# Kernel tuning notes

Measured on AMD Instinct MI355X. Metric: run time of the kernel, lower is better.

Reference implementation:

```python
import jax, jax.numpy as jnp
import numpy as np

BS, N, DE, DX = 16, 256, 64, 256
BIG = 100000.0


def setup_inputs() -> dict:
    key = jax.random.key(0)
    k1, k2, k3, k4 = jax.random.split(key, 4)
    E = jax.random.normal(k1, (BS, N, N, DE), dtype=jnp.float32)
    e_mask2 = jax.random.uniform(k2, (BS, 1, N, 1)) < 0.8
    fan_in = 4 * DE
    bound = 1.0 / np.sqrt(fan_in)
    W = jax.random.uniform(k3, (DX, fan_in), minval=-bound, maxval=bound, dtype=jnp.float32)
    b = jax.random.uniform(k4, (DX,), minval=-bound, maxval=bound, dtype=jnp.float32)
    return {"E": E, "e_mask2": e_mask2, "W": W, "b": b}


def reference(E, e_mask2, W, b):
    bs, n, _, de = E.shape
    mask = jnp.broadcast_to(e_mask2, (bs, n, n, de)).astype(E.dtype)  # bs,n,n,de
    imask = 1.0 - mask
    denom = mask.sum(axis=2)                       # bs,n,de
    m = E.sum(axis=2) / denom                      # (faithful: unmasked sum / mask count)
    mi = (E + BIG * imask).min(axis=2)             # masked min
    ma = (E - BIG * imask).max(axis=2)             # masked max
    std = (((E - m[:, :, None, :]) ** 2) * mask).sum(axis=2) / denom
    z = jnp.concatenate((m, mi, ma, std), axis=2)  # bs,n,4*de
    return jnp.einsum('bnf,df->bnd', z, W) + b     # bs,n,dx
```

## Files before the change

### kernel.cpp

```cpp
#include <hip/hip_runtime.h>
#include <cstdint>
#include <cstddef>

#define BSZ 16
#define NN  256
#define DE  64
#define DXX 256
#define FAN (4 * DE)
#define IB  4
#define RB  16

__global__ __launch_bounds__(256) void prep_kernel(
    const uint8_t* __restrict__ raw, const float* __restrict__ W,
    float* __restrict__ WT, float* __restrict__ maskf)
{
    const int t   = threadIdx.x;
    const int blk = blockIdx.x;
    if (blk < FAN) {
        WT[blk * DXX + t] = W[t * FAN + blk];
    } else {
        __shared__ int det[2];
        if (t == 0) { det[0] = 0; det[1] = 0; }
        __syncthreads();
        int s1 = 0, s23 = 0;
        const uint8_t* p = raw + t * 16;
        #pragma unroll
        for (int u = 0; u < 16; ++u) {
            int v = (int)p[u];
            int m4 = u & 3;
            if (m4 == 1) s1 += v; else if (m4 >= 2) s23 += v;
        }
        if (s1)  atomicAdd(&det[0], s1);
        if (s23) atomicAdd(&det[1], s23);
        __syncthreads();
        const int kind = (det[1] == 0) ? 1 : ((det[0] == 0) ? 2 : 0);
        for (int idx = t; idx < BSZ * NN; idx += 256) {
            float mv;
            if (kind == 1)      mv = (((const int*)(const void*)raw)[idx] != 0) ? 1.f : 0.f;
            else if (kind == 2) mv = (((const float*)(const void*)raw)[idx] != 0.f) ? 1.f : 0.f;
            else                mv = (raw[idx] != 0) ? 1.f : 0.f;
            maskf[idx] = mv;
        }
    }
}

__global__ __launch_bounds__(256, 4) void k1_stats(
    const float* __restrict__ E, const float* __restrict__ maskf,
    float* __restrict__ zout)
{
    __shared__ float m_lds[NN];
    __shared__ float cpart[4];
    __shared__ float partial[4][16][20];

    const int t    = threadIdx.x;
    const int g0   = blockIdx.x * IB;
    const int b    = g0 >> 8;
    const int wv   = t >> 6;
    const int lane = t & 63;

    float mv = maskf[b * NN + t];
    m_lds[t] = mv;
    unsigned long long bal = __ballot(mv != 0.f);
    if (lane == 0) cpart[wv] = (float)__popcll(bal);
    __syncthreads();
    const float inv_cnt = 1.0f / (cpart[0] + cpart[1] + cpart[2] + cpart[3]);

    const int dq = t & 15;
    const int jb = t >> 4;

    float mk[16];
    #pragma unroll
    for (int k = 0; k < 16; ++k) mk[k] = m_lds[jb + 16 * k];

    const float* base0 = E + (size_t)g0 * (NN * DE) + (size_t)jb * DE + 4 * dq;

    #define LD(P, K) (*(const float4*)((P) + (size_t)(K) * (16 * DE)))
    float4 A0, A1, A2, A3, B0, B1, B2, B3;
    A0 = LD(base0, 0); A1 = LD(base0, 1); A2 = LD(base0, 2); A3 = LD(base0, 3);

    for (int r = 0; r < IB; ++r) {
        const float* baser = base0 + (size_t)r * (NN * DE);

        float s[4]  = {0.f, 0.f, 0.f, 0.f};
        float ms[4] = {0.f, 0.f, 0.f, 0.f};
        float q[4]  = {0.f, 0.f, 0.f, 0.f};
        float mi[4] = {1e30f, 1e30f, 1e30f, 1e30f};
        float ma[4] = {-1e30f, -1e30f, -1e30f, -1e30f};

        #define CONS1(V, KK) { \
            float mkv = mk[KK]; \
            bool on = (mkv != 0.f); \
            float4 v = V; \
            s[0] += v.x; s[1] += v.y; s[2] += v.z; s[3] += v.w; \
            ms[0] = fmaf(mkv, v.x, ms[0]); ms[1] = fmaf(mkv, v.y, ms[1]); \
            ms[2] = fmaf(mkv, v.z, ms[2]); ms[3] = fmaf(mkv, v.w, ms[3]); \
            q[0] = fmaf(mkv * v.x, v.x, q[0]); q[1] = fmaf(mkv * v.y, v.y, q[1]); \
            q[2] = fmaf(mkv * v.z, v.z, q[2]); q[3] = fmaf(mkv * v.w, v.w, q[3]); \
            mi[0] = fminf(mi[0], on ? v.x : 1e30f); mi[1] = fminf(mi[1], on ? v.y : 1e30f); \
            mi[2] = fminf(mi[2], on ? v.z : 1e30f); mi[3] = fminf(mi[3], on ? v.w : 1e30f); \
            ma[0] = fmaxf(ma[0], on ? v.x : -1e30f); ma[1] = fmaxf(ma[1], on ? v.y : -1e30f); \
            ma[2] = fmaxf(ma[2], on ? v.z : -1e30f); ma[3] = fmaxf(ma[3], on ? v.w : -1e30f); \
        }

        B0 = LD(baser, 4);  B1 = LD(baser, 5);  B2 = LD(baser, 6);  B3 = LD(baser, 7);
        CONS1(A0, 0) CONS1(A1, 1) CONS1(A2, 2) CONS1(A3, 3)
        A0 = LD(baser, 8);  A1 = LD(baser, 9);  A2 = LD(baser, 10); A3 = LD(baser, 11);
        CONS1(B0, 4) CONS1(B1, 5) CONS1(B2, 6) CONS1(B3, 7)
        B0 = LD(baser, 12); B1 = LD(baser, 13); B2 = LD(baser, 14); B3 = LD(baser, 15);
        CONS1(A0, 8) CONS1(A1, 9) CONS1(A2, 10) CONS1(A3, 11)
        if (r < IB - 1) {
            const float* basen = baser + (NN * DE);
            A0 = LD(basen, 0); A1 = LD(basen, 1); A2 = LD(basen, 2); A3 = LD(basen, 3);
        }
        CONS1(B0, 12) CONS1(B1, 13) CONS1(B2, 14) CONS1(B3, 15)
        #undef CONS1

        #pragma unroll
        for (int c = 0; c < 4; ++c) {
            s[c]  += __shfl_xor(s[c], 16);  s[c]  += __shfl_xor(s[c], 32);
            ms[c] += __shfl_xor(ms[c], 16); ms[c] += __shfl_xor(ms[c], 32);
            q[c]  += __shfl_xor(q[c], 16);  q[c]  += __shfl_xor(q[c], 32);
            mi[c] = fminf(mi[c], __shfl_xor(mi[c], 16));
            mi[c] = fminf(mi[c], __shfl_xor(mi[c], 32));
            ma[c] = fmaxf(ma[c], __shfl_xor(ma[c], 16));
            ma[c] = fmaxf(ma[c], __shfl_xor(ma[c], 32));
        }

        if (lane < 16) {
            float* p = partial[wv][lane];
            #pragma unroll
            for (int c = 0; c < 4; ++c) {
                p[c]      = s[c];
                p[4 + c]  = ms[c];
                p[8 + c]  = q[c];
                p[12 + c] = mi[c];
                p[16 + c] = ma[c];
            }
        }
        __syncthreads();

        if (t < 64) {
            const int d = t, dq2 = d >> 2, c = d & 3;
            float ss = 0.f, mss = 0.f, mq = 0.f, lmi = 1e30f, lma = -1e30f;
            #pragma unroll
            for (int w = 0; w < 4; ++w) {
                const float* p = partial[w][dq2];
                ss  += p[c];
                mss += p[4 + c];
                mq  += p[8 + c];
                lmi  = fminf(lmi, p[12 + c]);
                lma  = fmaxf(lma, p[16 + c]);
            }
            float m    = ss * inv_cnt;
            float stdv = mq * inv_cnt - 2.0f * m * (mss * inv_cnt) + m * m;
            float* zr = zout + (size_t)(g0 + r) * FAN;
            zr[d]       = m;
            zr[64 + d]  = lmi;
            zr[128 + d] = lma;
            zr[192 + d] = stdv;
        }
        __syncthreads();
    }
    #undef LD
}

__global__ __launch_bounds__(256, 2) void k2_gemm(
    const float* __restrict__ zin, const float* __restrict__ WT,
    const float* __restrict__ bias, float* __restrict__ out)
{
    __shared__ float  z_s[RB][FAN];
    __shared__ float4 part_c[4][RB][64];

    const int t    = threadIdx.x;
    const int r0   = blockIdx.x * RB;
    const int wv   = t >> 6;
    const int lane = t & 63;

    #pragma unroll
    for (int i = 0; i < RB; ++i)
        z_s[i][t] = zin[(size_t)(r0 + i) * FAN + t];
    __syncthreads();

    float4 acc[RB];
    #pragma unroll
    for (int i = 0; i < RB; ++i) acc[i] = make_float4(0.f, 0.f, 0.f, 0.f);

    const float4* WT4 = (const float4*)WT;
    int f0 = 64 * wv;
    #pragma unroll 2
    for (int fg = 0; fg < 16; ++fg, f0 += 4) {
        float4 w0 = WT4[(size_t)(f0 + 0) * 64 + lane];
        float4 w1 = WT4[(size_t)(f0 + 1) * 64 + lane];
        float4 w2 = WT4[(size_t)(f0 + 2) * 64 + lane];
        float4 w3 = WT4[(size_t)(f0 + 3) * 64 + lane];
        #pragma unroll
        for (int i = 0; i < RB; ++i) {
            float4 z4 = *(const float4*)(&z_s[i][f0]);
            acc[i].x = fmaf(z4.x, w0.x, fmaf(z4.y, w1.x, fmaf(z4.z, w2.x, fmaf(z4.w, w3.x, acc[i].x))));
            acc[i].y = fmaf(z4.x, w0.y, fmaf(z4.y, w1.y, fmaf(z4.z, w2.y, fmaf(z4.w, w3.y, acc[i].y))));
            acc[i].z = fmaf(z4.x, w0.z, fmaf(z4.y, w1.z, fmaf(z4.z, w2.z, fmaf(z4.w, w3.z, acc[i].z))));
            acc[i].w = fmaf(z4.x, w0.w, fmaf(z4.y, w1.w, fmaf(z4.z, w2.w, fmaf(z4.w, w3.w, acc[i].w))));
        }
    }
    #pragma unroll
    for (int i = 0; i < RB; ++i) part_c[wv][i][lane] = acc[i];
    __syncthreads();

    #pragma unroll
    for (int pass = 0; pass < 4; ++pass) {
        const int idx = pass * 256 + t;
        const int row = idx >> 6, l2 = idx & 63;
        float4 p0 = part_c[0][row][l2], p1 = part_c[1][row][l2];
        float4 p2 = part_c[2][row][l2], p3 = part_c[3][row][l2];
        float4 bv = *(const float4*)(bias + 4 * l2);
        float4 o;
        o.x = p0.x + p1.x + p2.x + p3.x + bv.x;
        o.y = p0.y + p1.y + p2.y + p3.y + bv.y;
        o.z = p0.z + p1.z + p2.z + p3.z + bv.z;
        o.w = p0.w + p1.w + p2.w + p3.w + bv.w;
        *(float4*)(out + (size_t)(r0 + row) * DXX + 4 * l2) = o;
    }
}

__global__ __launch_bounds__(256, 4) void etox_legacy(
    const float* __restrict__ E, const uint8_t* __restrict__ raw,
    const float* __restrict__ W, const float* __restrict__ bias,
    float* __restrict__ out)
{
    __shared__ float m_lds[NN];
    __shared__ int   det[2];
    __shared__ float cpart[4];
    __shared__ float partial[4][16][20];
    __shared__ float z_lds[IB][FAN];

    const int t    = threadIdx.x;
    const int g0   = blockIdx.x * IB;
    const int b    = g0 >> 8;
    const int wv   = t >> 6;
    const int lane = t & 63;

    if (t == 0) { det[0] = 0; det[1] = 0; }
    int s1 = 0, s23 = 0;
    {
        const uint8_t* p = raw + t * 16;
        #pragma unroll
        for (int u = 0; u < 16; ++u) {
            int v = (int)p[u];
            int m4 = u & 3;
            if (m4 == 1) s1 += v; else if (m4 >= 2) s23 += v;
        }
    }
    __syncthreads();
    if (s1)  atomicAdd(&det[0], s1);
    if (s23) atomicAdd(&det[1], s23);
    __syncthreads();
    const int kind = (det[1] == 0) ? 1 : ((det[0] == 0) ? 2 : 0);
    float mv;
    {
        int idx = b * NN + t;
        if (kind == 1)      mv = (((const int*)(const void*)raw)[idx] != 0) ? 1.f : 0.f;
        else if (kind == 2) mv = (((const float*)(const void*)raw)[idx] != 0.f) ? 1.f : 0.f;
        else                mv = (raw[idx] != 0) ? 1.f : 0.f;
    }
    m_lds[t] = mv;
    unsigned long long bal = __ballot(mv != 0.f);
    if (lane == 0) cpart[wv] = (float)__popcll(bal);
    __syncthreads();
    const float inv_cnt = 1.0f / (cpart[0] + cpart[1] + cpart[2] + cpart[3]);

    const int dq = t & 15;
    const int jb = t >> 4;
    const float* base0 = E + (size_t)g0 * (NN * DE) + (size_t)jb * DE + 4 * dq;

    #define LD(P, K) (*(const float4*)((P) + (size_t)(K) * (16 * DE)))
    float4 A0, A1, A2, A3, B0, B1, B2, B3;
    A0 = LD(base0, 0); A1 = LD(base0, 1); A2 = LD(base0, 2); A3 = LD(base0, 3);

    for (int r = 0; r < IB; ++r) {
        const float* baser = base0 + (size_t)r * (NN * DE);
        float s[4]  = {0.f, 0.f, 0.f, 0.f};
        float ms[4] = {0.f, 0.f, 0.f, 0.f};
        float q[4]  = {0.f, 0.f, 0.f, 0.f};
        float mi[4] = {1e30f, 1e30f, 1e30f, 1e30f};
        float ma[4] = {-1e30f, -1e30f, -1e30f, -1e30f};

        #define CONS1(V, KK) { \
            float mkv = m_lds[jb + 16 * (KK)]; \
            bool on = (mkv != 0.f); \
            float4 v = V; \
            s[0] += v.x; s[1] += v.y; s[2] += v.z; s[3] += v.w; \
            ms[0] = fmaf(mkv, v.x, ms[0]); ms[1] = fmaf(mkv, v.y, ms[1]); \
            ms[2] = fmaf(mkv, v.z, ms[2]); ms[3] = fmaf(mkv, v.w, ms[3]); \
            q[0] = fmaf(mkv * v.x, v.x, q[0]); q[1] = fmaf(mkv * v.y, v.y, q[1]); \
            q[2] = fmaf(mkv * v.z, v.z, q[2]); q[3] = fmaf(mkv * v.w, v.w, q[3]); \
            mi[0] = fminf(mi[0], on ? v.x : 1e30f); mi[1] = fminf(mi[1], on ? v.y : 1e30f); \
            mi[2] = fminf(mi[2], on ? v.z : 1e30f); mi[3] = fminf(mi[3], on ? v.w : 1e30f); \
            ma[0] = fmaxf(ma[0], on ? v.x : -1e30f); ma[1] = fmaxf(ma[1], on ? v.y : -1e30f); \
            ma[2] = fmaxf(ma[2], on ? v.z : -1e30f); ma[3] = fmaxf(ma[3], on ? v.w : -1e30f); \
        }

        B0 = LD(baser, 4);  B1 = LD(baser, 5);  B2 = LD(baser, 6);  B3 = LD(baser, 7);
        CONS1(A0, 0) CONS1(A1, 1) CONS1(A2, 2) CONS1(A3, 3)
        A0 = LD(baser, 8);  A1 = LD(baser, 9);  A2 = LD(baser, 10); A3 = LD(baser, 11);
        CONS1(B0, 4) CONS1(B1, 5) CONS1(B2, 6) CONS1(B3, 7)
        B0 = LD(baser, 12); B1 = LD(baser, 13); B2 = LD(baser, 14); B3 = LD(baser, 15);
        CONS1(A0, 8) CONS1(A1, 9) CONS1(A2, 10) CONS1(A3, 11)
        if (r < IB - 1) {
            const float* basen = baser + (NN * DE);
            A0 = LD(basen, 0); A1 = LD(basen, 1); A2 = LD(basen, 2); A3 = LD(basen, 3);
        }
        CONS1(B0, 12) CONS1(B1, 13) CONS1(B2, 14) CONS1(B3, 15)
        #undef CONS1

        #pragma unroll
        for (int c = 0; c < 4; ++c) {
            s[c]  += __shfl_xor(s[c], 16);  s[c]  += __shfl_xor(s[c], 32);
            ms[c] += __shfl_xor(ms[c], 16); ms[c] += __shfl_xor(ms[c], 32);
            q[c]  += __shfl_xor(q[c], 16);  q[c]  += __shfl_xor(q[c], 32);
            mi[c] = fminf(mi[c], __shfl_xor(mi[c], 16));
            mi[c] = fminf(mi[c], __shfl_xor(mi[c], 32));
            ma[c] = fmaxf(ma[c], __shfl_xor(ma[c], 16));
            ma[c] = fmaxf(ma[c], __shfl_xor(ma[c], 32));
        }

        if (lane < 16) {
            float* p = partial[wv][lane];
            #pragma unroll
            for (int c = 0; c < 4; ++c) {
                p[c] = s[c]; p[4+c] = ms[c]; p[8+c] = q[c];
                p[12+c] = mi[c]; p[16+c] = ma[c];
            }
        }
        __syncthreads();

        if (t < 64) {
            const int d = t, dq2 = d >> 2, c = d & 3;
            float ss = 0.f, mss = 0.f, mq = 0.f, lmi = 1e30f, lma = -1e30f;
            #pragma unroll
            for (int w = 0; w < 4; ++w) {
                const float* p = partial[w][dq2];
                ss += p[c]; mss += p[4+c]; mq += p[8+c];
                lmi = fminf(lmi, p[12+c]); lma = fmaxf(lma, p[16+c]);
            }
            float m    = ss * inv_cnt;
            float stdv = mq * inv_cnt - 2.0f * m * (mss * inv_cnt) + m * m;
            z_lds[r][d] = m; z_lds[r][64+d] = lmi; z_lds[r][128+d] = lma; z_lds[r][192+d] = stdv;
        }
        __syncthreads();
    }
    #undef LD

    float acc0, acc1, acc2, acc3;
    {
        float bv = bias[t];
        acc0 = bv; acc1 = bv; acc2 = bv; acc3 = bv;
    }
    const float4* Wrow = (const float4*)(W + (size_t)t * FAN);
    #pragma unroll 8
    for (int f4 = 0; f4 < 64; ++f4) {
        float4 w4 = Wrow[f4];
        int f = 4 * f4;
        acc0 += z_lds[0][f]*w4.x + z_lds[0][f+1]*w4.y + z_lds[0][f+2]*w4.z + z_lds[0][f+3]*w4.w;
        acc1 += z_lds[1][f]*w4.x + z_lds[1][f+1]*w4.y + z_lds[1][f+2]*w4.z + z_lds[1][f+3]*w4.w;
        acc2 += z_lds[2][f]*w4.x + z_lds[2][f+1]*w4.y + z_lds[2][f+2]*w4.z + z_lds[2][f+3]*w4.w;
        acc3 += z_lds[3][f]*w4.x + z_lds[3][f+1]*w4.y + z_lds[3][f+2]*w4.z + z_lds[3][f+3]*w4.w;
    }
    out[(size_t)(g0 + 0) * DXX + t] = acc0;
    out[(size_t)(g0 + 1) * DXX + t] = acc1;
    out[(size_t)(g0 + 2) * DXX + t] = acc2;
    out[(size_t)(g0 + 3) * DXX + t] = acc3;
}

extern "C" void kernel_launch(void* const* d_in, const int* in_sizes, int n_in,
                              void* d_out, int out_size, void* d_ws, size_t ws_size,
                              hipStream_t stream) {
    const float*   E    = (const float*)d_in[0];
    const uint8_t* mraw = (const uint8_t*)d_in[1];
    const float*   W    = (const float*)d_in[2];
    const float*   bias = (const float*)d_in[3];
    float*         out  = (float*)d_out;

    const size_t wt_n   = (size_t)FAN * DXX;
    const size_t mask_n = (size_t)BSZ * NN;
    const size_t z_n    = (size_t)BSZ * NN * FAN;
    const size_t need   = (wt_n + mask_n + z_n) * sizeof(float);

    if (ws_size >= need) {
        float* WT    = (float*)d_ws;
        float* maskf = WT + wt_n;
        float* zbuf  = maskf + mask_n;
        prep_kernel<<<FAN + 1, 256, 0, stream>>>(mraw, W, WT, maskf);
        k1_stats<<<(BSZ * NN) / IB, 256, 0, stream>>>(E, maskf, zbuf);
        k2_gemm<<<(BSZ * NN) / RB, 256, 0, stream>>>(zbuf, WT, bias, out);
    } else {
        etox_legacy<<<(BSZ * NN) / IB, 256, 0, stream>>>(E, mraw, W, bias, out);
    }
}
```

Before: 77.54 us.

## Fuse stats and GEMM into one producer-consumer kernel with a GEMV warp

Merges the stats kernel and the separate GEMM kernel into a single kernel with 320 threads: four waves compute the per-row statistics into LDS while a fifth consumer wave computes the matrix-vector product for the previous row, overlapping the two stages. This removes the global round-trip of the z buffer and one kernel launch. In exchange, every block re-reads the full transposed weight matrix (256 KB) from cache per row instead of amortizing it over 16 rows. Mask values are now read from LDS per element rather than held in registers.

```diff
diff --git a/kernel.cpp b/kernel.cpp
--- a/kernel.cpp
+++ b/kernel.cpp
@@ -8,7 +8,6 @@
 #define DXX 256
 #define FAN (4 * DE)
 #define IB  4
-#define RB  16
 
 __global__ __launch_bounds__(256) void prep_kernel(
     const uint8_t* __restrict__ raw, const float* __restrict__ W,
@@ -44,98 +43,124 @@
     }
 }
 
-__global__ __launch_bounds__(256, 4) void k1_stats(
+__global__ __launch_bounds__(320, 5) void etox_pc(
     const float* __restrict__ E, const float* __restrict__ maskf,
-    float* __restrict__ zout)
+    const float* __restrict__ WT, const float* __restrict__ bias,
+    float* __restrict__ out)
 {
     __shared__ float m_lds[NN];
     __shared__ float cpart[4];
     __shared__ float partial[4][16][20];
-
-    const int t    = threadIdx.x;
-    const int g0   = blockIdx.x * IB;
-    const int b    = g0 >> 8;
-    const int wv   = t >> 6;
-    const int lane = t & 63;
-
-    float mv = maskf[b * NN + t];
-    m_lds[t] = mv;
-    unsigned long long bal = __ballot(mv != 0.f);
-    if (lane == 0) cpart[wv] = (float)__popcll(bal);
+    __shared__ float z_lds[IB][FAN];
+
+    const int t      = threadIdx.x;
+    const int g0     = blockIdx.x * IB;
+    const int b      = g0 >> 8;
+    const int wv     = t >> 6;
+    const int lane   = t & 63;
+    const bool cons  = (t >= 256);
+
+    if (!cons) {
+        float mv = maskf[b * NN + t];
+        m_lds[t] = mv;
+        unsigned long long bal = __ballot(mv != 0.f);
+        if (lane == 0) cpart[wv] = (float)__popcll(bal);
+    }
     __syncthreads();
     const float inv_cnt = 1.0f / (cpart[0] + cpart[1] + cpart[2] + cpart[3]);
 
+    const float4* WT4 = (const float4*)WT;
+    float4 bv4 = make_float4(0.f, 0.f, 0.f, 0.f);
+    if (cons) bv4 = *(const float4*)(bias + 4 * lane);
+
     const int dq = t & 15;
     const int jb = t >> 4;
-
-    float mk[16];
-    #pragma unroll
-    for (int k = 0; k < 16; ++k) mk[k] = m_lds[jb + 16 * k];
-
     const float* base0 = E + (size_t)g0 * (NN * DE) + (size_t)jb * DE + 4 * dq;
 
     #define LD(P, K) (*(const float4*)((P) + (size_t)(K) * (16 * DE)))
     float4 A0, A1, A2, A3, B0, B1, B2, B3;
-    A0 = LD(base0, 0); A1 = LD(base0, 1); A2 = LD(base0, 2); A3 = LD(base0, 3);
+    if (!cons) { A0 = LD(base0, 0); A1 = LD(base0, 1); A2 = LD(base0, 2); A3 = LD(base0, 3); }
+
+    #define CONS_MV(RZ, DEST_ROW) { \
+        float4 acc = make_float4(0.f, 0.f, 0.f, 0.f); \
+        _Pragma("unroll 4") \
+        for (int f = 0; f < FAN; f += 4) { \
+            float4 w0 = WT4[(size_t)(f + 0) * 64 + lane]; \
+            float4 w1 = WT4[(size_t)(f + 1) * 64 + lane]; \
+            float4 w2 = WT4[(size_t)(f + 2) * 64 + lane]; \
+            float4 w3 = WT4[(size_t)(f + 3) * 64 + lane]; \
+            float4 z4 = *(const float4*)(&z_lds[RZ][f]); \
+            acc.x = fmaf(z4.x, w0.x, fmaf(z4.y, w1.x, fmaf(z4.z, w2.x, fmaf(z4.w, w3.x, acc.x)))); \
+            acc.y = fmaf(z4.x, w0.y, fmaf(z4.y, w1.y, fmaf(z4.z, w2.y, fmaf(z4.w, w3.y, acc.y)))); \
+            acc.z = fmaf(z4.x, w0.z, fmaf(z4.y, w1.z, fmaf(z4.z, w2.z, fmaf(z4.w, w3.z, acc.z)))); \
+            acc.w = fmaf(z4.x, w0.w, fmaf(z4.y, w1.w, fmaf(z4.z, w2.w, fmaf(z4.w, w3.w, acc.w)))); \
+        } \
+        acc.x += bv4.x; acc.y += bv4.y; acc.z += bv4.z; acc.w += bv4.w; \
+        *(float4*)(out + (size_t)(g0 + (DEST_ROW)) * DXX + 4 * lane) = acc; \
+    }
 
     for (int r = 0; r < IB; ++r) {
-        const float* baser = base0 + (size_t)r * (NN * DE);
-
-        float s[4]  = {0.f, 0.f, 0.f, 0.f};
-        float ms[4] = {0.f, 0.f, 0.f, 0.f};
-        float q[4]  = {0.f, 0.f, 0.f, 0.f};
-        float mi[4] = {1e30f, 1e30f, 1e30f, 1e30f};
-        float ma[4] = {-1e30f, -1e30f, -1e30f, -1e30f};
-
-        #define CONS1(V, KK) { \
-            float mkv = mk[KK]; \
-            bool on = (mkv != 0.f); \
-            float4 v = V; \
-            s[0] += v.x; s[1] += v.y; s[2] += v.z; s[3] += v.w; \
-            ms[0] = fmaf(mkv, v.x, ms[0]); ms[1] = fmaf(mkv, v.y, ms[1]); \
-            ms[2] = fmaf(mkv, v.z, ms[2]); ms[3] = fmaf(mkv, v.w, ms[3]); \
-            q[0] = fmaf(mkv * v.x, v.x, q[0]); q[1] = fmaf(mkv * v.y, v.y, q[1]); \
-            q[2] = fmaf(mkv * v.z, v.z, q[2]); q[3] = fmaf(mkv * v.w, v.w, q[3]); \
-            mi[0] = fminf(mi[0], on ? v.x : 1e30f); mi[1] = fminf(mi[1], on ? v.y : 1e30f); \
-            mi[2] = fminf(mi[2], on ? v.z : 1e30f); mi[3] = fminf(mi[3], on ? v.w : 1e30f); \
-            ma[0] = fmaxf(ma[0], on ? v.x : -1e30f); ma[1] = fmaxf(ma[1], on ? v.y : -1e30f); \
-            ma[2] = fmaxf(ma[2], on ? v.z : -1e30f); ma[3] = fmaxf(ma[3], on ? v.w : -1e30f); \
-        }
-
-        B0 = LD(baser, 4);  B1 = LD(baser, 5);  B2 = LD(baser, 6);  B3 = LD(baser, 7);
-        CONS1(A0, 0) CONS1(A1, 1) CONS1(A2, 2) CONS1(A3, 3)
-        A0 = LD(baser, 8);  A1 = LD(baser, 9);  A2 = LD(baser, 10); A3 = LD(baser, 11);
-        CONS1(B0, 4) CONS1(B1, 5) CONS1(B2, 6) CONS1(B3, 7)
-        B0 = LD(baser, 12); B1 = LD(baser, 13); B2 = LD(baser, 14); B3 = LD(baser, 15);
-        CONS1(A0, 8) CONS1(A1, 9) CONS1(A2, 10) CONS1(A3, 11)
-        if (r < IB - 1) {
-            const float* basen = baser + (NN * DE);
-            A0 = LD(basen, 0); A1 = LD(basen, 1); A2 = LD(basen, 2); A3 = LD(basen, 3);
-        }
-        CONS1(B0, 12) CONS1(B1, 13) CONS1(B2, 14) CONS1(B3, 15)
-        #undef CONS1
-
-        #pragma unroll
-        for (int c = 0; c < 4; ++c) {
-            s[c]  += __shfl_xor(s[c], 16);  s[c]  += __shfl_xor(s[c], 32);
-            ms[c] += __shfl_xor(ms[c], 16); ms[c] += __shfl_xor(ms[c], 32);
-            q[c]  += __shfl_xor(q[c], 16);  q[c]  += __shfl_xor(q[c], 32);
-            mi[c] = fminf(mi[c], __shfl_xor(mi[c], 16));
-            mi[c] = fminf(mi[c], __shfl_xor(mi[c], 32));
-            ma[c] = fmaxf(ma[c], __shfl_xor(ma[c], 16));
-            ma[c] = fmaxf(ma[c], __shfl_xor(ma[c], 32));
-        }
-
-        if (lane < 16) {
-            float* p = partial[wv][lane];
+        if (!cons) {
+            const float* baser = base0 + (size_t)r * (NN * DE);
+
+            float s[4]  = {0.f, 0.f, 0.f, 0.f};
+            float ms[4] = {0.f, 0.f, 0.f, 0.f};
+            float q[4]  = {0.f, 0.f, 0.f, 0.f};
+            float mi[4] = {1e30f, 1e30f, 1e30f, 1e30f};
+            float ma[4] = {-1e30f, -1e30f, -1e30f, -1e30f};
+
+            #define CONS1(V, KK) { \
+                float mk = m_lds[jb + 16 * (KK)]; \
+                bool on = (mk != 0.f); \
+                float4 v = V; \
+                s[0] += v.x; s[1] += v.y; s[2] += v.z; s[3] += v.w; \
+                ms[0] = fmaf(mk, v.x, ms[0]); ms[1] = fmaf(mk, v.y, ms[1]); \
+                ms[2] = fmaf(mk, v.z, ms[2]); ms[3] = fmaf(mk, v.w, ms[3]); \
+                q[0] = fmaf(mk * v.x, v.x, q[0]); q[1] = fmaf(mk * v.y, v.y, q[1]); \
+                q[2] = fmaf(mk * v.z, v.z, q[2]); q[3] = fmaf(mk * v.w, v.w, q[3]); \
+                mi[0] = fminf(mi[0], on ? v.x : 1e30f); mi[1] = fminf(mi[1], on ? v.y : 1e30f); \
+                mi[2] = fminf(mi[2], on ? v.z : 1e30f); mi[3] = fminf(mi[3], on ? v.w : 1e30f); \
+                ma[0] = fmaxf(ma[0], on ? v.x : -1e30f); ma[1] = fmaxf(ma[1], on ? v.y : -1e30f); \
+                ma[2] = fmaxf(ma[2], on ? v.z : -1e30f); ma[3] = fmaxf(ma[3], on ? v.w : -1e30f); \
+            }
+
+            B0 = LD(baser, 4);  B1 = LD(baser, 5);  B2 = LD(baser, 6);  B3 = LD(baser, 7);
+            CONS1(A0, 0) CONS1(A1, 1) CONS1(A2, 2) CONS1(A3, 3)
+            A0 = LD(baser, 8);  A1 = LD(baser, 9);  A2 = LD(baser, 10); A3 = LD(baser, 11);
+            CONS1(B0, 4) CONS1(B1, 5) CONS1(B2, 6) CONS1(B3, 7)
+            B0 = LD(baser, 12); B1 = LD(baser, 13); B2 = LD(baser, 14); B3 = LD(baser, 15);
+            CONS1(A0, 8) CONS1(A1, 9) CONS1(A2, 10) CONS1(A3, 11)
+            if (r < IB - 1) {
+                const float* basen = baser + (NN * DE);
+                A0 = LD(basen, 0); A1 = LD(basen, 1); A2 = LD(basen, 2); A3 = LD(basen, 3);
+            }
+            CONS1(B0, 12) CONS1(B1, 13) CONS1(B2, 14) CONS1(B3, 15)
+            #undef CONS1
+
             #pragma unroll
             for (int c = 0; c < 4; ++c) {
-                p[c]      = s[c];
-                p[4 + c]  = ms[c];
-                p[8 + c]  = q[c];
-                p[12 + c] = mi[c];
-                p[16 + c] = ma[c];
-            }
+                s[c]  += __shfl_xor(s[c], 16);  s[c]  += __shfl_xor(s[c], 32);
+                ms[c] += __shfl_xor(ms[c], 16); ms[c] += __shfl_xor(ms[c], 32);
+                q[c]  += __shfl_xor(q[c], 16);  q[c]  += __shfl_xor(q[c], 32);
+                mi[c] = fminf(mi[c], __shfl_xor(mi[c], 16));
+                mi[c] = fminf(mi[c], __shfl_xor(mi[c], 32));
+                ma[c] = fmaxf(ma[c], __shfl_xor(ma[c], 16));
+                ma[c] = fmaxf(ma[c], __shfl_xor(ma[c], 32));
+            }
+
+            if (lane < 16) {
+                float* p = partial[wv][lane];
+                #pragma unroll
+                for (int c = 0; c < 4; ++c) {
+                    p[c]      = s[c];
+                    p[4 + c]  = ms[c];
+                    p[8 + c]  = q[c];
+                    p[12 + c] = mi[c];
+                    p[16 + c] = ma[c];
+                }
+            }
+        } else {
+            if (r > 0) CONS_MV(r - 1, r - 1)
         }
         __syncthreads();
 
@@ -153,73 +178,17 @@
             }
             float m    = ss * inv_cnt;
             float stdv = mq * inv_cnt - 2.0f * m * (mss * inv_cnt) + m * m;
-            float* zr = zout + (size_t)(g0 + r) * FAN;
-            zr[d]       = m;
-            zr[64 + d]  = lmi;
-            zr[128 + d] = lma;
-            zr[192 + d] = stdv;
+            z_lds[r][d]       = m;
+            z_lds[r][64 + d]  = lmi;
+            z_lds[r][128 + d] = lma;
+            z_lds[r][192 + d] = stdv;
         }
         __syncthreads();
     }
     #undef LD
-}
-
-__global__ __launch_bounds__(256, 2) void k2_gemm(
-    const float* __restrict__ zin, const float* __restrict__ WT,
-    const float* __restrict__ bias, float* __restrict__ out)
-{
-    __shared__ float  z_s[RB][FAN];
-    __shared__ float4 part_c[4][RB][64];
-
-    const int t    = threadIdx.x;
-    const int r0   = blockIdx.x * RB;
-    const int wv   = t >> 6;
-    const int lane = t & 63;
-
-    #pragma unroll
-    for (int i = 0; i < RB; ++i)
-        z_s[i][t] = zin[(size_t)(r0 + i) * FAN + t];
-    __syncthreads();
-
-    float4 acc[RB];
-    #pragma unroll
-    for (int i = 0; i < RB; ++i) acc[i] = make_float4(0.f, 0.f, 0.f, 0.f);
-
-    const float4* WT4 = (const float4*)WT;
-    int f0 = 64 * wv;
-    #pragma unroll 2
-    for (int fg = 0; fg < 16; ++fg, f0 += 4) {
-        float4 w0 = WT4[(size_t)(f0 + 0) * 64 + lane];
-        float4 w1 = WT4[(size_t)(f0 + 1) * 64 + lane];
-        float4 w2 = WT4[(size_t)(f0 + 2) * 64 + lane];
-        float4 w3 = WT4[(size_t)(f0 + 3) * 64 + lane];
-        #pragma unroll
-        for (int i = 0; i < RB; ++i) {
-            float4 z4 = *(const float4*)(&z_s[i][f0]);
-            acc[i].x = fmaf(z4.x, w0.x, fmaf(z4.y, w1.x, fmaf(z4.z, w2.x, fmaf(z4.w, w3.x, acc[i].x))));
-            acc[i].y = fmaf(z4.x, w0.y, fmaf(z4.y, w1.y, fmaf(z4.z, w2.y, fmaf(z4.w, w3.y, acc[i].y))));
-            acc[i].z = fmaf(z4.x, w0.z, fmaf(z4.y, w1.z, fmaf(z4.z, w2.z, fmaf(z4.w, w3.z, acc[i].z))));
-            acc[i].w = fmaf(z4.x, w0.w, fmaf(z4.y, w1.w, fmaf(z4.z, w2.w, fmaf(z4.w, w3.w, acc[i].w))));
-        }
-    }
-    #pragma unroll
-    for (int i = 0; i < RB; ++i) part_c[wv][i][lane] = acc[i];
-    __syncthreads();
-
-    #pragma unroll
-    for (int pass = 0; pass < 4; ++pass) {
-        const int idx = pass * 256 + t;
-        const int row = idx >> 6, l2 = idx & 63;
-        float4 p0 = part_c[0][row][l2], p1 = part_c[1][row][l2];
-        float4 p2 = part_c[2][row][l2], p3 = part_c[3][row][l2];
-        float4 bv = *(const float4*)(bias + 4 * l2);
-        float4 o;
-        o.x = p0.x + p1.x + p2.x + p3.x + bv.x;
-        o.y = p0.y + p1.y + p2.y + p3.y + bv.y;
-        o.z = p0.z + p1.z + p2.z + p3.z + bv.z;
-        o.w = p0.w + p1.w + p2.w + p3.w + bv.w;
-        *(float4*)(out + (size_t)(r0 + row) * DXX + 4 * l2) = o;
-    }
+
+    if (cons) CONS_MV(IB - 1, IB - 1)
+    #undef CONS_MV
 }
 
 __global__ __launch_bounds__(256, 4) void etox_legacy(
@@ -382,16 +351,13 @@
 
     const size_t wt_n   = (size_t)FAN * DXX;
     const size_t mask_n = (size_t)BSZ * NN;
-    const size_t z_n    = (size_t)BSZ * NN * FAN;
-    const size_t need   = (wt_n + mask_n + z_n) * sizeof(float);
+    const size_t need   = (wt_n + mask_n) * sizeof(float);
 
     if (ws_size >= need) {
         float* WT    = (float*)d_ws;
         float* maskf = WT + wt_n;
-        float* zbuf  = maskf + mask_n;
         prep_kernel<<<FAN + 1, 256, 0, stream>>>(mraw, W, WT, maskf);
-        k1_stats<<<(BSZ * NN) / IB, 256, 0, stream>>>(E, maskf, zbuf);
-        k2_gemm<<<(BSZ * NN) / RB, 256, 0, stream>>>(zbuf, WT, bias, out);
+        etox_pc<<<(BSZ * NN) / IB, 320, 0, stream>>>(E, maskf, WT, bias, out);
     } else {
         etox_legacy<<<(BSZ * NN) / IB, 256, 0, stream>>>(E, mraw, W, bias, out);
     }
```

After: 168.4 us. 2.17x slower.
